# Performance work log

Measured on AMD Instinct MI355X. Metric: run time of the kernel, lower is better.

## Reference

```python
import jax, jax.numpy as jnp
import numpy as np

# --- cfg constants (from init_kwargs) ---
T = 100
DT_MS = 1.0
MAX_RATE_HZ = 200.0
TAU_MEM = 20.0
TAU_PRE = 20.0
TAU_POST = 20.0
V_TH = 16.0
LR_POST = 0.01
LR_PRE = 0.012
W_MAX = 1.0
B, F, N_IN = 256, 1024, 784


def setup_inputs() -> dict:
    key = jax.random.key(0)
    k1, k2, k3 = jax.random.split(key, 3)
    image = jax.random.uniform(k1, (B, 1, 28, 28), dtype=jnp.float32)
    noise = jax.random.uniform(k2, (T, B, 1, 28, 28), dtype=jnp.float32)
    # non-negative excitatory weights, kernel 28x28 flattened -> (F, 784)
    W = jax.random.uniform(k3, (F, N_IN), dtype=jnp.float32) * 0.3
    return {"image": image, "W": W, "noise": noise}


def reference(image, W, noise):
    """Returns spike_count: (B, n_filters)."""
    b = image.shape[0]
    f = W.shape[0]
    # Poisson encoding: P(spike at t) = rate*dt = image * max_rate_hz * dt_ms/1000
    p = image.reshape(b, -1) * (MAX_RATE_HZ * DT_MS / 1000.0)        # (B, 784)
    spikes_in = (noise.reshape(T, b, -1) < p[None]).astype(jnp.float32)  # (T, B, 784)

    decay_mem = jnp.float32(np.exp(-DT_MS / TAU_MEM))
    decay_pre = jnp.float32(np.exp(-DT_MS / TAU_PRE))
    decay_post = jnp.float32(np.exp(-DT_MS / TAU_POST))

    def step(carry, pre):
        mem, w, apre, apost, cnt = carry
        # conv with 28x28 kernel, padding 0 == FC: (B,784) @ (784,F)
        I = pre @ w.T                                   # (B, F)
        mem = mem * decay_mem + I
        spk = (mem >= V_TH).astype(mem.dtype)           # LIF threshold
        mem = mem * (1.0 - spk)                         # reset to 0 on spike
        # --- STDP (pair-based, batch-averaged, Diehl & Cook style) ---
        apre = apre * decay_pre + pre                   # (B, 784) pre trace
        dw_plus = (LR_POST / b) * jnp.einsum('bf,bi->fi', spk, apre)   # LTP on post spike
        dw_minus = (LR_PRE / b) * jnp.einsum('bf,bi->fi', apost, pre)  # LTD on pre spike
        w = jnp.clip(w + dw_plus - dw_minus, 0.0, W_MAX)
        apost = apost * decay_post + spk                # (B, F) post trace
        cnt = cnt + spk
        return (mem, w, apre, apost, cnt), None

    init = (jnp.zeros((b, f), jnp.float32),   # mem
            W,                                 # plastic weights
            jnp.zeros((b, N_IN), jnp.float32), # apre
            jnp.zeros((b, f), jnp.float32),    # apost
            jnp.zeros((b, f), jnp.float32))    # spike_count
    (mem, w, apre, apost, cnt), _ = jax.lax.scan(step, init, spikes_in)
    return cnt
```

## Files before the change

### kernel.cpp

```cpp
#include <hip/hip_runtime.h>
#include <math.h>

#define TSTEPS 100
#define BB 256
#define FF 1024
#define NIN 784
#define NW 13
#define CAPA 192
#define CAPB 128
#define NBLK 1024
#define TPB 256
#define BARSZ 17408

typedef unsigned long long u64;
typedef float f4 __attribute__((ext_vector_type(4)));

__device__ __forceinline__ unsigned at_ld(unsigned* p) {
    return __hip_atomic_load(p, __ATOMIC_RELAXED, __HIP_MEMORY_SCOPE_AGENT);
}
__device__ __forceinline__ void at_st(unsigned* p, unsigned v) {
    __hip_atomic_store(p, v, __ATOMIC_RELAXED, __HIP_MEMORY_SCOPE_AGENT);
}
__device__ __forceinline__ u64 at_ld64(u64* p) {
    return __hip_atomic_load(p, __ATOMIC_RELAXED, __HIP_MEMORY_SCOPE_AGENT);
}
__device__ __forceinline__ void at_st64(u64* p, u64 v) {
    __hip_atomic_store(p, v, __ATOMIC_RELAXED, __HIP_MEMORY_SCOPE_AGENT);
}

__device__ __forceinline__ float sc0_ld(const float* p) {
    float v;
    asm volatile("global_load_dword %0, %1, off sc0\n\t"
                 "s_waitcnt vmcnt(0)"
                 : "=v"(v) : "v"(p) : "memory");
    __builtin_amdgcn_sched_barrier(0);
    return v;
}
__device__ __forceinline__ f4 sc0_ld4(const f4* p) {
    f4 v;
    asm volatile("global_load_dwordx4 %0, %1, off sc0\n\t"
                 "s_waitcnt vmcnt(0)"
                 : "=v"(v) : "v"(p) : "memory");
    __builtin_amdgcn_sched_barrier(0);
    return v;
}
__device__ __forceinline__ void sc0_issue8(
    const float* p0, const float* p1, const float* p2, const float* p3,
    const float* p4, const float* p5, const float* p6, const float* p7,
    float& v0, float& v1, float& v2, float& v3,
    float& v4, float& v5, float& v6, float& v7)
{
    asm volatile(
        "global_load_dword %0, %8, off sc0\n\t"
        "global_load_dword %1, %9, off sc0\n\t"
        "global_load_dword %2, %10, off sc0\n\t"
        "global_load_dword %3, %11, off sc0\n\t"
        "global_load_dword %4, %12, off sc0\n\t"
        "global_load_dword %5, %13, off sc0\n\t"
        "global_load_dword %6, %14, off sc0\n\t"
        "global_load_dword %7, %15, off sc0"
        : "=&v"(v0),"=&v"(v1),"=&v"(v2),"=&v"(v3),
          "=&v"(v4),"=&v"(v5),"=&v"(v6),"=&v"(v7)
        : "v"(p0),"v"(p1),"v"(p2),"v"(p3),"v"(p4),"v"(p5),"v"(p6),"v"(p7)
        : "memory");
}
__device__ __forceinline__ void sc0_ld8(
    const float* p0, const float* p1, const float* p2, const float* p3,
    const float* p4, const float* p5, const float* p6, const float* p7,
    float& v0, float& v1, float& v2, float& v3,
    float& v4, float& v5, float& v6, float& v7)
{
    sc0_issue8(p0,p1,p2,p3,p4,p5,p6,p7, v0,v1,v2,v3,v4,v5,v6,v7);
    asm volatile("s_waitcnt vmcnt(0)" ::: "memory");
    __builtin_amdgcn_sched_barrier(0);
}

template <typename IDX>
__device__ __forceinline__ float foldList(
    const float* __restrict__ base, const IDX* __restrict__ list,
    int k0, int k1, int f)
{
    float c = 0.f;
    int k = k0;
    for (; k + 16 <= k1; k += 16) {
        float v0,v1,v2,v3,v4,v5,v6,v7,v8,v9,v10,v11,v12,v13,v14,v15;
        sc0_issue8(base+((int)list[k+0]<<10)+f, base+((int)list[k+1]<<10)+f,
                   base+((int)list[k+2]<<10)+f, base+((int)list[k+3]<<10)+f,
                   base+((int)list[k+4]<<10)+f, base+((int)list[k+5]<<10)+f,
                   base+((int)list[k+6]<<10)+f, base+((int)list[k+7]<<10)+f,
                   v0,v1,v2,v3,v4,v5,v6,v7);
        sc0_issue8(base+((int)list[k+8]<<10)+f,  base+((int)list[k+9]<<10)+f,
                   base+((int)list[k+10]<<10)+f, base+((int)list[k+11]<<10)+f,
                   base+((int)list[k+12]<<10)+f, base+((int)list[k+13]<<10)+f,
                   base+((int)list[k+14]<<10)+f, base+((int)list[k+15]<<10)+f,
                   v8,v9,v10,v11,v12,v13,v14,v15);
        asm volatile("s_waitcnt vmcnt(0)" ::: "memory");
        __builtin_amdgcn_sched_barrier(0);
        c=__fadd_rn(c,v0);  c=__fadd_rn(c,v1);  c=__fadd_rn(c,v2);  c=__fadd_rn(c,v3);
        c=__fadd_rn(c,v4);  c=__fadd_rn(c,v5);  c=__fadd_rn(c,v6);  c=__fadd_rn(c,v7);
        c=__fadd_rn(c,v8);  c=__fadd_rn(c,v9);  c=__fadd_rn(c,v10); c=__fadd_rn(c,v11);
        c=__fadd_rn(c,v12); c=__fadd_rn(c,v13); c=__fadd_rn(c,v14); c=__fadd_rn(c,v15);
    }
    if (k + 8 <= k1) {
        float v0,v1,v2,v3,v4,v5,v6,v7;
        sc0_ld8(base+((int)list[k+0]<<10)+f, base+((int)list[k+1]<<10)+f,
                base+((int)list[k+2]<<10)+f, base+((int)list[k+3]<<10)+f,
                base+((int)list[k+4]<<10)+f, base+((int)list[k+5]<<10)+f,
                base+((int)list[k+6]<<10)+f, base+((int)list[k+7]<<10)+f,
                v0,v1,v2,v3,v4,v5,v6,v7);
        c=__fadd_rn(c,v0); c=__fadd_rn(c,v1); c=__fadd_rn(c,v2); c=__fadd_rn(c,v3);
        c=__fadd_rn(c,v4); c=__fadd_rn(c,v5); c=__fadd_rn(c,v6); c=__fadd_rn(c,v7);
        k += 8;
    }
    for (; k < k1; ++k)
        c = __fadd_rn(c, sc0_ld(base + ((int)list[k] << 10) + f));
    return c;
}

__global__ __launch_bounds__(256) void k_init(
    const float* __restrict__ W, float* __restrict__ wT,
    float* __restrict__ apreT_g, u64* __restrict__ spkT,
    unsigned* __restrict__ bar)
{
    int idx = blockIdx.x * 256 + threadIdx.x;
    {
        int f = idx & (FF - 1);
        int i = idx >> 10;
        wT[idx] = W[f * NIN + i];
    }
    apreT_g[idx] = 0.f;
    apreT_g[idx + NIN * FF] = 0.f;
    if (idx < 2 * FF * 4) spkT[idx] = 0ull;
    if (idx < BARSZ) bar[idx] = 0u;
}

__global__ __launch_bounds__(256) void k_encode(
    const float* __restrict__ image, const float* __restrict__ noise,
    u64* __restrict__ prebits)
{
    int tid = blockIdx.x * 256 + threadIdx.x;
    int lane = threadIdx.x & 63;
    int word = tid >> 6;
    int wd = word % NW;
    int tb = word / NW;
    int b = tb & (BB - 1);
    int i = (wd << 6) + lane;
    bool s = false;
    if (i < NIN) {
        float pf = __fmul_rn(image[b * NIN + i], 0.2f);
        s = (noise[(size_t)tb * NIN + i] < pf);
    }
    u64 m = __ballot(s);
    if (lane == 0) prebits[word] = m;
}

__global__ __launch_bounds__(256) void k_encode_t(
    const u64* __restrict__ prebits, u64* __restrict__ prebitsT)
{
    int tid = blockIdx.x * 256 + threadIdx.x;
    int b = tid & (BB - 1);
    int ti = tid >> 8;
    int i = ti % NIN;
    int t = ti / NIN;
    u64 w = prebits[((size_t)t * BB + b) * NW + (i >> 6)];
    bool s = (w >> (i & 63)) & 1ull;
    u64 m = __ballot(s);
    if ((threadIdx.x & 63) == 0)
        prebitsT[(size_t)ti * 4 + ((threadIdx.x >> 6) & 3)] = m;
}

__global__ __launch_bounds__(256) void k_lists(
    const u64* __restrict__ prebits, unsigned short* __restrict__ idxA,
    unsigned short* __restrict__ cntA)
{
    int tb = blockIdx.x * 256 + threadIdx.x;
    const u64* pb = prebits + (size_t)tb * NW;
    unsigned short* ia = idxA + (size_t)tb * CAPA;
    int n = 0, c1 = 0, c2 = 0;
    for (int wd = 0; wd < NW; ++wd) {
        u64 m = pb[wd];
        int boff = wd << 6;
        while (m) {
            int j = __builtin_ctzll(m); m &= m - 1;
            if (n < CAPA) ia[n] = (unsigned short)(boff + j);
            ++n;
        }
        if (wd == 5)  c1 = n;
        if (wd == 11) c2 = n;
    }
    if (n > CAPA) n = CAPA;
    if (c2 > n) c2 = n;
    if (c1 > c2) c1 = c2;
    cntA[tb * 4 + 0] = (unsigned short)c1;
    cntA[tb * 4 + 1] = (unsigned short)c2;
    cntA[tb * 4 + 2] = (unsigned short)n;
}

__global__ __launch_bounds__(256) void k_listsT(
    const u64* __restrict__ prebitsT, unsigned char* __restrict__ idxB,
    unsigned short* __restrict__ cntB)
{
    int ti = blockIdx.x * 256 + threadIdx.x;
    if (ti >= TSTEPS * NIN) return;
    const u64* pt = prebitsT + (size_t)ti * 4;
    unsigned char* ib = idxB + (size_t)ti * CAPB;
    int n = 0;
    for (int wb = 0; wb < 4; ++wb) {
        u64 m = pt[wb];
        int boff = wb << 6;
        while (m) {
            int j = __builtin_ctzll(m); m &= m - 1;
            if (n < CAPB) ib[n] = (unsigned char)(boff + j);
            ++n;
        }
    }
    cntB[ti] = (unsigned short)(n > CAPB ? CAPB : n);
}

__global__ __launch_bounds__(TPB, 4) void k_run(
    float* __restrict__ wT, float* __restrict__ apreT_g, float* __restrict__ apost,
    const unsigned short* __restrict__ idxA, const unsigned short* __restrict__ cntA,
    const unsigned char* __restrict__ idxB, const unsigned short* __restrict__ cntB,
    const u64* __restrict__ prebitsT, u64* __restrict__ spkT,
    float* __restrict__ out, unsigned* __restrict__ bar,
    float dmem, float dpre, float dpost, float lrp, float lrm)
{
    __shared__ int shs[16];
    __shared__ int shinfo[4];
    __shared__ unsigned scnt[9];
    __shared__ int sbad;
    __shared__ float sap[4][256];

    const int tix = threadIdx.x;
    const int wv = tix >> 6, lane = tix & 63;
    const int bid = blockIdx.x;

    unsigned* slot = bar;
    if (tix < 9) scnt[tix] = 0u;
    if (tix == 0) {
        unsigned x;
        asm volatile("s_getreg_b32 %0, hwreg(HW_REG_XCC_ID)" : "=s"(x));
        shinfo[0] = (int)(x & 7u);
        at_st(&slot[bid], (x & 7u) + 1u);
    }
    __syncthreads();
    const int xcd = shinfo[0];
    unsigned mv0, mv1, mv2, mv3;
    for (int rounds = 0;; ++rounds) {
        if (tix == 0) sbad = 0;
        __syncthreads();
        mv0 = at_ld(&slot[tix]);
        mv1 = at_ld(&slot[256 + tix]);
        mv2 = at_ld(&slot[512 + tix]);
        mv3 = at_ld(&slot[768 + tix]);
        if (!(mv0 && mv1 && mv2 && mv3)) sbad = 1;
        __syncthreads();
        if (!sbad || rounds > (1 << 20)) break;
        __builtin_amdgcn_s_sleep(2);
    }
    {
        atomicAdd(&scnt[mv0 - 1u], 1u);
        atomicAdd(&scnt[mv1 - 1u], 1u);
        atomicAdd(&scnt[mv2 - 1u], 1u);
        atomicAdd(&scnt[mv3 - 1u], 1u);
        unsigned r = 0;
        if ((int)(mv0 - 1u) == xcd && tix < bid) r++;
        if ((int)(mv1 - 1u) == xcd && 256 + tix < bid) r++;
        if ((int)(mv2 - 1u) == xcd && 512 + tix < bid) r++;
        if ((int)(mv3 - 1u) == xcd && 768 + tix < bid) r++;
        if (r) atomicAdd(&scnt[8], r);
        __syncthreads();
        if (tix == 0) {
            int Kn = 0, gidx = 0;
            for (int x2 = 0; x2 < 8; ++x2)
                if (scnt[x2] > 0) { if (x2 == xcd) gidx = Kn; ++Kn; }
            int ns = 0;
            for (int s = 0; s < 16; ++s)
                if ((s % Kn) == gidx) shs[ns++] = s;
            shinfo[1] = (int)scnt[8];
            shinfo[2] = (int)scnt[xcd];
            shinfo[3] = ns;
        }
        __syncthreads();
    }
    const int rank = shinfo[1], nx = shinfo[2], nsl = shinfo[3];
    const int nxw = nx * 4;
    const int wrank = rank * 4 + wv;
    const int nA = nsl << 8;
    const int nB = nsl * NIN;
    float* apx = apreT_g + (size_t)xcd * (BB * NIN);
    float* sapw = sap[wv];
    unsigned* arrive  = bar + 1024 + xcd * 1024;
    unsigned* release = bar + 9216 + xcd * 1024;
    unsigned ep = 1;

#define A_STATE(Q) float memv##Q = 0.f, cntv##Q = 0.f, apov##Q = 0.f; u64 pbal##Q = 0ull;
    A_STATE(0) A_STATE(1) A_STATE(2) A_STATE(3)

#define DO_A(Q) do { \
    int u = wrank + (Q) * nxw; \
    if (u < nA) { \
        int sl = u >> 8, b = u & 255; \
        int f = (shs[sl] << 6) + lane; \
        apov##Q = __fadd_rn(__fmul_rn(apov##Q, dpost), \
                            (float)((pbal##Q >> lane) & 1ull)); \
        apost[(b << 10) + f] = apov##Q; \
        const unsigned short* ia = idxA + (size_t)(t * BB + b) * CAPA; \
        const unsigned short* ca = cntA + (size_t)(t * BB + b) * 4; \
        int c1 = ca[0], c2 = ca[1], c3 = ca[2]; \
        float I = 0.f; \
        I = __fadd_rn(I, foldList(wT, ia, 0,  c1, f)); \
        I = __fadd_rn(I, foldList(wT, ia, c1, c2, f)); \
        I = __fadd_rn(I, foldList(wT, ia, c2, c3, f)); \
        float mm = __fadd_rn(__fmul_rn(memv##Q, dmem), I); \
        bool spk = (mm >= 16.0f); \
        memv##Q = spk ? 0.f : mm; \
        if (spk) { \
            cntv##Q += 1.f; \
            atomicOr(&cur[(f << 2) | (b >> 6)], 1ull << (b & 63)); \
        } \
        pbal##Q = __ballot(spk); \
    } \
} while (0)

    auto xbar = [&]() {
        asm volatile("s_waitcnt vmcnt(0) lgkmcnt(0)" ::: "memory");
        __syncthreads();
        if (rank == 0) {
            for (int rounds = 0;; ++rounds) {
                if (tix == 0) sbad = 0;
                __syncthreads();
                bool ok = true;
                #pragma unroll
                for (int kk = 0; kk < 4; ++kk) {
                    int r = kk * 256 + tix;
                    if (r < nx && r > 0) ok &= (at_ld(&arrive[r]) >= ep);
                }
                if (!ok) sbad = 1;
                __syncthreads();
                if (!sbad || rounds > (1 << 20)) break;
                __builtin_amdgcn_s_sleep(4);
            }
            #pragma unroll
            for (int kk = 0; kk < 4; ++kk) {
                int r = kk * 256 + tix;
                if (r < nx) at_st(&release[r], ep);
            }
        } else {
            if (tix == 0) {
                at_st(&arrive[rank], ep);
                unsigned spins = 0;
                while (at_ld(&release[rank]) < ep) {
                    if (++spins > (1u << 22)) break;
                    __builtin_amdgcn_s_sleep(8);
                }
            }
            __syncthreads();
        }
        ++ep;
    };

    for (int t = 0; t < TSTEPS; ++t) {
        u64* cur = spkT + (size_t)(t & 1) * (FF * 4);
        u64* nxt = spkT + (size_t)((t + 1) & 1) * (FF * 4);

        DO_A(0); DO_A(1); DO_A(2); DO_A(3);

        for (int r = wrank; r < NIN; r += nxw) {
            const u64* pt = prebitsT + ((size_t)t * NIN + r) * 4;
            u64 w0 = pt[0], w1 = pt[1], w2 = pt[2], w3 = pt[3];
            int bb = lane << 2;
            u64 wsel = (bb & 128) ? ((bb & 64) ? w3 : w2)
                                  : ((bb & 64) ? w1 : w0);
            int s0 = bb & 63;
            f4* vp = (f4*)(apx + ((size_t)r << 8) + bb);
            f4 v = *vp;
            v.x = __fadd_rn(__fmul_rn(v.x, dpre), (float)((wsel >> s0) & 1ull));
            v.y = __fadd_rn(__fmul_rn(v.y, dpre), (float)((wsel >> (s0+1)) & 1ull));
            v.z = __fadd_rn(__fmul_rn(v.z, dpre), (float)((wsel >> (s0+2)) & 1ull));
            v.w = __fadd_rn(__fmul_rn(v.w, dpre), (float)((wsel >> (s0+3)) & 1ull));
            *vp = v;
        }
        for (int wd0 = rank * TPB + tix; wd0 < (nsl << 8); wd0 += nx * TPB) {
            int sl = wd0 >> 8, rest = wd0 & 255;
            int f = (shs[sl] << 6) + (rest >> 2);
            at_st64(&nxt[(f << 2) + (rest & 3)], 0ull);
        }

        if (t == TSTEPS - 1) break;
        xbar();

        for (int q = 0;; ++q) {
            int u = wrank + q * nxw;
            if (u >= nB) break;
            int sl = u / NIN, i = u - sl * NIN;
            int f = (shs[sl] << 6) + lane;

            const unsigned char* ib = idxB + (size_t)(t * NIN + i) * CAPB;
            int cb = cntB[t * NIN + i];
            float Sm = foldList(apost, ib, 0, cb, f);

            asm volatile("s_waitcnt lgkmcnt(0)" ::: "memory");
            __builtin_amdgcn_sched_barrier(0);
            f4 rv = sc0_ld4((const f4*)(apx + ((size_t)i << 8) + (lane << 2)));
            *(f4*)(sapw + (lane << 2)) = rv;
            u64 m0 = at_ld64(&cur[(f << 2) | 0]);
            u64 m1 = at_ld64(&cur[(f << 2) | 1]);
            u64 m2 = at_ld64(&cur[(f << 2) | 2]);
            u64 m3 = at_ld64(&cur[(f << 2) | 3]);
            asm volatile("s_waitcnt lgkmcnt(0)" ::: "memory");
            __builtin_amdgcn_sched_barrier(0);

            float Sp = 0.f;
            u64 m;
            m = m0; while (m) { int j = __builtin_ctzll(m); m &= m - 1;
                                Sp = __fadd_rn(Sp, sapw[j]); }
            m = m1; while (m) { int j = __builtin_ctzll(m); m &= m - 1;
                                Sp = __fadd_rn(Sp, sapw[64 + j]); }
            m = m2; while (m) { int j = __builtin_ctzll(m); m &= m - 1;
                                Sp = __fadd_rn(Sp, sapw[128 + j]); }
            m = m3; while (m) { int j = __builtin_ctzll(m); m &= m - 1;
                                Sp = __fadd_rn(Sp, sapw[192 + j]); }

            int wi = (i << 10) + f;
            float w = wT[wi];
            w = __fadd_rn(w, __fmul_rn(lrp, Sp));
            w = __fsub_rn(w, __fmul_rn(lrm, Sm));
            w = fminf(fmaxf(w, 0.f), 1.f);
            wT[wi] = w;
        }
        xbar();
    }

#define DO_OUT(Q) do { \
    int u = wrank + (Q) * nxw; \
    if (u < nA) { \
        int sl = u >> 8, b = u & 255; \
        int f = (shs[sl] << 6) + lane; \
        out[(b << 10) + f] = cntv##Q; \
    } \
} while (0)
    DO_OUT(0); DO_OUT(1); DO_OUT(2); DO_OUT(3);
}

extern "C" void kernel_launch(void* const* d_in, const int* in_sizes, int n_in,
                              void* d_out, int out_size, void* d_ws, size_t ws_size,
                              hipStream_t stream)
{
    const float* image = (const float*)d_in[0];
    const float* W     = (const float*)d_in[1];
    const float* noise = (const float*)d_in[2];
    float* out = (float*)d_out;

    char* p = (char*)d_ws;
    float* wT      = (float*)p; p += (size_t)NIN * FF * 4;
    float* apreT_g = (float*)p; p += (size_t)8 * BB * NIN * 4;
    float* apost   = (float*)p; p += (size_t)BB * FF * 4;
    u64* prebits   = (u64*)p;   p += (size_t)TSTEPS * BB * NW * 8;
    u64* prebitsT  = (u64*)p;   p += (size_t)TSTEPS * NIN * 4 * 8;
    u64* spkT      = (u64*)p;   p += (size_t)2 * FF * 4 * 8;
    unsigned short* idxA = (unsigned short*)p; p += (size_t)TSTEPS * BB * CAPA * 2;
    unsigned short* cntA = (unsigned short*)p; p += (size_t)TSTEPS * BB * 4 * 2;
    unsigned char*  idxB = (unsigned char*)p;  p += (size_t)TSTEPS * NIN * CAPB;
    unsigned short* cntB = (unsigned short*)p; p += (size_t)TSTEPS * NIN * 2;
    unsigned* bar        = (unsigned*)p;       p += (size_t)BARSZ * 4;

    float dmem = (float)exp(-1.0 / 20.0);
    float dpre = dmem, dpost = dmem;
    float lrp = (float)(0.01 / 256.0);
    float lrm = (float)(0.012 / 256.0);

    k_init<<<(NIN * FF) / 256, 256, 0, stream>>>(W, wT, apreT_g, spkT, bar);
    k_encode<<<(TSTEPS * BB * NW * 64) / 256, 256, 0, stream>>>(image, noise, prebits);
    k_encode_t<<<(TSTEPS * NIN * BB) / 256, 256, 0, stream>>>(prebits, prebitsT);
    k_lists<<<(TSTEPS * BB) / 256, 256, 0, stream>>>(prebits, idxA, cntA);
    k_listsT<<<(TSTEPS * NIN + 255) / 256, 256, 0, stream>>>(prebitsT, idxB, cntB);

    k_run<<<NBLK, TPB, 0, stream>>>(
        wT, apreT_g, apost, idxA, cntA, idxB, cntB,
        prebitsT, spkT, out, bar, dmem, dpre, dpost, lrp, lrm);
}
```

Measured before the change: 4.842 ms.

## Replace atomicOr spike bitmaps with per-wave ballot stores and in-register transpose

```diff
diff --git a/kernel.cpp b/kernel.cpp
--- a/kernel.cpp
+++ b/kernel.cpp
@@ -8,9 +8,9 @@
 #define NW 13
 #define CAPA 192
 #define CAPB 128
-#define NBLK 1024
-#define TPB 256
-#define BARSZ 17408
+#define NBLK 512
+#define TPB 512
+#define BARSZ 8704
 
 typedef unsigned long long u64;
 typedef float f4 __attribute__((ext_vector_type(4)));
@@ -19,12 +19,6 @@
     return __hip_atomic_load(p, __ATOMIC_RELAXED, __HIP_MEMORY_SCOPE_AGENT);
 }
 __device__ __forceinline__ void at_st(unsigned* p, unsigned v) {
-    __hip_atomic_store(p, v, __ATOMIC_RELAXED, __HIP_MEMORY_SCOPE_AGENT);
-}
-__device__ __forceinline__ u64 at_ld64(u64* p) {
-    return __hip_atomic_load(p, __ATOMIC_RELAXED, __HIP_MEMORY_SCOPE_AGENT);
-}
-__device__ __forceinline__ void at_st64(u64* p, u64 v) {
     __hip_atomic_store(p, v, __ATOMIC_RELAXED, __HIP_MEMORY_SCOPE_AGENT);
 }
 
@@ -43,6 +37,20 @@
                  : "=v"(v) : "v"(p) : "memory");
     __builtin_amdgcn_sched_barrier(0);
     return v;
+}
+__device__ __forceinline__ void sc0_ld64x4(
+    const u64* p0, const u64* p1, const u64* p2, const u64* p3,
+    u64& a, u64& b, u64& c, u64& d)
+{
+    asm volatile(
+        "global_load_dwordx2 %0, %4, off sc0\n\t"
+        "global_load_dwordx2 %1, %5, off sc0\n\t"
+        "global_load_dwordx2 %2, %6, off sc0\n\t"
+        "global_load_dwordx2 %3, %7, off sc0\n\t"
+        "s_waitcnt vmcnt(0)"
+        : "=&v"(a),"=&v"(b),"=&v"(c),"=&v"(d)
+        : "v"(p0),"v"(p1),"v"(p2),"v"(p3) : "memory");
+    __builtin_amdgcn_sched_barrier(0);
 }
 __device__ __forceinline__ void sc0_issue8(
     const float* p0, const float* p1, const float* p2, const float* p3,
@@ -119,8 +127,7 @@
 
 __global__ __launch_bounds__(256) void k_init(
     const float* __restrict__ W, float* __restrict__ wT,
-    float* __restrict__ apreT_g, u64* __restrict__ spkT,
-    unsigned* __restrict__ bar)
+    float* __restrict__ apreT_g, unsigned* __restrict__ bar)
 {
     int idx = blockIdx.x * 256 + threadIdx.x;
     {
@@ -130,7 +137,6 @@
     }
     apreT_g[idx] = 0.f;
     apreT_g[idx + NIN * FF] = 0.f;
-    if (idx < 2 * FF * 4) spkT[idx] = 0ull;
     if (idx < BARSZ) bar[idx] = 0u;
 }
 
@@ -217,26 +223,26 @@
     cntB[ti] = (unsigned short)(n > CAPB ? CAPB : n);
 }
 
-__global__ __launch_bounds__(TPB, 4) void k_run(
+__global__ __launch_bounds__(TPB, 2) void k_run(
     float* __restrict__ wT, float* __restrict__ apreT_g, float* __restrict__ apost,
     const unsigned short* __restrict__ idxA, const unsigned short* __restrict__ cntA,
     const unsigned char* __restrict__ idxB, const unsigned short* __restrict__ cntB,
-    const u64* __restrict__ prebitsT, u64* __restrict__ spkT,
+    const u64* __restrict__ prebitsT, u64* __restrict__ spkb,
     float* __restrict__ out, unsigned* __restrict__ bar,
     float dmem, float dpre, float dpost, float lrp, float lrm)
 {
     __shared__ int shs[16];
     __shared__ int shinfo[4];
-    __shared__ unsigned scnt[9];
+    __shared__ unsigned scnt[16];
     __shared__ int sbad;
-    __shared__ float sap[4][256];
+    __shared__ float sap[8][256];
 
     const int tix = threadIdx.x;
     const int wv = tix >> 6, lane = tix & 63;
     const int bid = blockIdx.x;
 
     unsigned* slot = bar;
-    if (tix < 9) scnt[tix] = 0u;
+    if (tix < 16) scnt[tix] = 0u;
     if (tix == 0) {
         unsigned x;
         asm volatile("s_getreg_b32 %0, hwreg(HW_REG_XCC_ID)" : "=s"(x));
@@ -245,53 +251,40 @@
     }
     __syncthreads();
     const int xcd = shinfo[0];
-    unsigned mv0, mv1, mv2, mv3;
+    unsigned mv = 0;
     for (int rounds = 0;; ++rounds) {
         if (tix == 0) sbad = 0;
         __syncthreads();
-        mv0 = at_ld(&slot[tix]);
-        mv1 = at_ld(&slot[256 + tix]);
-        mv2 = at_ld(&slot[512 + tix]);
-        mv3 = at_ld(&slot[768 + tix]);
-        if (!(mv0 && mv1 && mv2 && mv3)) sbad = 1;
+        mv = at_ld(&slot[tix]);
+        if (!mv) sbad = 1;
         __syncthreads();
         if (!sbad || rounds > (1 << 20)) break;
         __builtin_amdgcn_s_sleep(2);
     }
-    {
-        atomicAdd(&scnt[mv0 - 1u], 1u);
-        atomicAdd(&scnt[mv1 - 1u], 1u);
-        atomicAdd(&scnt[mv2 - 1u], 1u);
-        atomicAdd(&scnt[mv3 - 1u], 1u);
-        unsigned r = 0;
-        if ((int)(mv0 - 1u) == xcd && tix < bid) r++;
-        if ((int)(mv1 - 1u) == xcd && 256 + tix < bid) r++;
-        if ((int)(mv2 - 1u) == xcd && 512 + tix < bid) r++;
-        if ((int)(mv3 - 1u) == xcd && 768 + tix < bid) r++;
-        if (r) atomicAdd(&scnt[8], r);
-        __syncthreads();
-        if (tix == 0) {
-            int Kn = 0, gidx = 0;
-            for (int x2 = 0; x2 < 8; ++x2)
-                if (scnt[x2] > 0) { if (x2 == xcd) gidx = Kn; ++Kn; }
-            int ns = 0;
-            for (int s = 0; s < 16; ++s)
-                if ((s % Kn) == gidx) shs[ns++] = s;
-            shinfo[1] = (int)scnt[8];
-            shinfo[2] = (int)scnt[xcd];
-            shinfo[3] = ns;
-        }
-        __syncthreads();
-    }
+    atomicAdd(&scnt[mv - 1u], 1u);
+    if ((int)(mv - 1u) == xcd && tix < bid) atomicAdd(&scnt[8], 1u);
+    __syncthreads();
+    if (tix == 0) {
+        int Kn = 0, gidx = 0;
+        for (int x2 = 0; x2 < 8; ++x2)
+            if (scnt[x2] > 0) { if (x2 == xcd) gidx = Kn; ++Kn; }
+        int ns = 0;
+        for (int s = 0; s < 16; ++s)
+            if ((s % Kn) == gidx) shs[ns++] = s;
+        shinfo[1] = (int)scnt[8];
+        shinfo[2] = (int)scnt[xcd];
+        shinfo[3] = ns;
+    }
+    __syncthreads();
     const int rank = shinfo[1], nx = shinfo[2], nsl = shinfo[3];
-    const int nxw = nx * 4;
-    const int wrank = rank * 4 + wv;
+    const int nxw = nx * 8;
+    const int wrank = rank * 8 + wv;
     const int nA = nsl << 8;
     const int nB = nsl * NIN;
     float* apx = apreT_g + (size_t)xcd * (BB * NIN);
     float* sapw = sap[wv];
-    unsigned* arrive  = bar + 1024 + xcd * 1024;
-    unsigned* release = bar + 9216 + xcd * 1024;
+    unsigned* arrive  = bar + 512 + xcd * 512;
+    unsigned* release = bar + 4608 + xcd * 512;
     unsigned ep = 1;
 
 #define A_STATE(Q) float memv##Q = 0.f, cntv##Q = 0.f, apov##Q = 0.f; u64 pbal##Q = 0ull;
@@ -301,7 +294,8 @@
     int u = wrank + (Q) * nxw; \
     if (u < nA) { \
         int sl = u >> 8, b = u & 255; \
-        int f = (shs[sl] << 6) + lane; \
+        int slice = shs[sl]; \
+        int f = (slice << 6) + lane; \
         apov##Q = __fadd_rn(__fmul_rn(apov##Q, dpost), \
                             (float)((pbal##Q >> lane) & 1ull)); \
         apost[(b << 10) + f] = apov##Q; \
@@ -315,11 +309,9 @@
         float mm = __fadd_rn(__fmul_rn(memv##Q, dmem), I); \
         bool spk = (mm >= 16.0f); \
         memv##Q = spk ? 0.f : mm; \
-        if (spk) { \
-            cntv##Q += 1.f; \
-            atomicOr(&cur[(f << 2) | (b >> 6)], 1ull << (b & 63)); \
-        } \
+        if (spk) cntv##Q += 1.f; \
         pbal##Q = __ballot(spk); \
+        if (lane == 0) spkb[(slice << 8) + b] = pbal##Q;    \
     } \
 } while (0)
 
@@ -330,22 +322,12 @@
             for (int rounds = 0;; ++rounds) {
                 if (tix == 0) sbad = 0;
                 __syncthreads();
-                bool ok = true;
-                #pragma unroll
-                for (int kk = 0; kk < 4; ++kk) {
-                    int r = kk * 256 + tix;
-                    if (r < nx && r > 0) ok &= (at_ld(&arrive[r]) >= ep);
-                }
-                if (!ok) sbad = 1;
+                if (tix > 0 && tix < nx && at_ld(&arrive[tix]) < ep) sbad = 1;
                 __syncthreads();
                 if (!sbad || rounds > (1 << 20)) break;
-                __builtin_amdgcn_s_sleep(4);
+                __builtin_amdgcn_s_sleep(1);
             }
-            #pragma unroll
-            for (int kk = 0; kk < 4; ++kk) {
-                int r = kk * 256 + tix;
-                if (r < nx) at_st(&release[r], ep);
-            }
+            if (tix < nx) at_st(&release[tix], ep);
         } else {
             if (tix == 0) {
                 at_st(&arrive[rank], ep);
@@ -361,9 +343,6 @@
     };
 
     for (int t = 0; t < TSTEPS; ++t) {
-        u64* cur = spkT + (size_t)(t & 1) * (FF * 4);
-        u64* nxt = spkT + (size_t)((t + 1) & 1) * (FF * 4);
-
         DO_A(0); DO_A(1); DO_A(2); DO_A(3);
 
         for (int r = wrank; r < NIN; r += nxw) {
@@ -381,46 +360,55 @@
             v.w = __fadd_rn(__fmul_rn(v.w, dpre), (float)((wsel >> (s0+3)) & 1ull));
             *vp = v;
         }
-        for (int wd0 = rank * TPB + tix; wd0 < (nsl << 8); wd0 += nx * TPB) {
-            int sl = wd0 >> 8, rest = wd0 & 255;
-            int f = (shs[sl] << 6) + (rest >> 2);
-            at_st64(&nxt[(f << 2) + (rest & 3)], 0ull);
-        }
 
         if (t == TSTEPS - 1) break;
         xbar();
 
+        int cursl = -1;
+        u64 tm0 = 0, tm1 = 0, tm2 = 0, tm3 = 0;
         for (int q = 0;; ++q) {
             int u = wrank + q * nxw;
             if (u >= nB) break;
             int sl = u / NIN, i = u - sl * NIN;
-            int f = (shs[sl] << 6) + lane;
+            int slice = shs[sl];
+            int f = (slice << 6) + lane;
+
+            if (sl != cursl) {
+                cursl = sl;
+                const u64* sb = spkb + (slice << 8);
+                u64 v0, v1, v2, v3;
+                sc0_ld64x4(sb + lane, sb + 64 + lane, sb + 128 + lane, sb + 192 + lane,
+                           v0, v1, v2, v3);
+                tm0 = tm1 = tm2 = tm3 = 0ull;
+                #pragma unroll 8
+                for (int fp = 0; fp < 64; ++fp) {
+                    u64 b0 = __ballot((int)((v0 >> fp) & 1ull));
+                    u64 b1 = __ballot((int)((v1 >> fp) & 1ull));
+                    u64 b2 = __ballot((int)((v2 >> fp) & 1ull));
+                    u64 b3 = __ballot((int)((v3 >> fp) & 1ull));
+                    if (lane == fp) { tm0 = b0; tm1 = b1; tm2 = b2; tm3 = b3; }
+                }
+            }
 
             const unsigned char* ib = idxB + (size_t)(t * NIN + i) * CAPB;
             int cb = cntB[t * NIN + i];
             float Sm = foldList(apost, ib, 0, cb, f);
 
+            f4 rv = sc0_ld4((const f4*)(apx + ((size_t)i << 8) + (lane << 2)));
+            *(f4*)(sapw + (lane << 2)) = rv;
             asm volatile("s_waitcnt lgkmcnt(0)" ::: "memory");
             __builtin_amdgcn_sched_barrier(0);
-            f4 rv = sc0_ld4((const f4*)(apx + ((size_t)i << 8) + (lane << 2)));
-            *(f4*)(sapw + (lane << 2)) = rv;
-            u64 m0 = at_ld64(&cur[(f << 2) | 0]);
-            u64 m1 = at_ld64(&cur[(f << 2) | 1]);
-            u64 m2 = at_ld64(&cur[(f << 2) | 2]);
-            u64 m3 = at_ld64(&cur[(f << 2) | 3]);
-            asm volatile("s_waitcnt lgkmcnt(0)" ::: "memory");
-            __builtin_amdgcn_sched_barrier(0);
 
             float Sp = 0.f;
             u64 m;
-            m = m0; while (m) { int j = __builtin_ctzll(m); m &= m - 1;
-                                Sp = __fadd_rn(Sp, sapw[j]); }
-            m = m1; while (m) { int j = __builtin_ctzll(m); m &= m - 1;
-                                Sp = __fadd_rn(Sp, sapw[64 + j]); }
-            m = m2; while (m) { int j = __builtin_ctzll(m); m &= m - 1;
-                                Sp = __fadd_rn(Sp, sapw[128 + j]); }
-            m = m3; while (m) { int j = __builtin_ctzll(m); m &= m - 1;
-                                Sp = __fadd_rn(Sp, sapw[192 + j]); }
+            m = tm0; while (m) { int j = __builtin_ctzll(m); m &= m - 1;
+                                 Sp = __fadd_rn(Sp, sapw[j]); }
+            m = tm1; while (m) { int j = __builtin_ctzll(m); m &= m - 1;
+                                 Sp = __fadd_rn(Sp, sapw[64 + j]); }
+            m = tm2; while (m) { int j = __builtin_ctzll(m); m &= m - 1;
+                                 Sp = __fadd_rn(Sp, sapw[128 + j]); }
+            m = tm3; while (m) { int j = __builtin_ctzll(m); m &= m - 1;
+                                 Sp = __fadd_rn(Sp, sapw[192 + j]); }
 
             int wi = (i << 10) + f;
             float w = wT[wi];
@@ -458,7 +446,7 @@
     float* apost   = (float*)p; p += (size_t)BB * FF * 4;
     u64* prebits   = (u64*)p;   p += (size_t)TSTEPS * BB * NW * 8;
     u64* prebitsT  = (u64*)p;   p += (size_t)TSTEPS * NIN * 4 * 8;
-    u64* spkT      = (u64*)p;   p += (size_t)2 * FF * 4 * 8;
+    u64* spkb      = (u64*)p;   p += (size_t)16 * 256 * 8;
     unsigned short* idxA = (unsigned short*)p; p += (size_t)TSTEPS * BB * CAPA * 2;
     unsigned short* cntA = (unsigned short*)p; p += (size_t)TSTEPS * BB * 4 * 2;
     unsigned char*  idxB = (unsigned char*)p;  p += (size_t)TSTEPS * NIN * CAPB;
@@ -470,7 +458,7 @@
     float lrp = (float)(0.01 / 256.0);
     float lrm = (float)(0.012 / 256.0);
 
-    k_init<<<(NIN * FF) / 256, 256, 0, stream>>>(W, wT, apreT_g, spkT, bar);
+    k_init<<<(NIN * FF) / 256, 256, 0, stream>>>(W, wT, apreT_g, bar);
     k_encode<<<(TSTEPS * BB * NW * 64) / 256, 256, 0, stream>>>(image, noise, prebits);
     k_encode_t<<<(TSTEPS * NIN * BB) / 256, 256, 0, stream>>>(prebits, prebitsT);
     k_lists<<<(TSTEPS * BB) / 256, 256, 0, stream>>>(prebits, idxA, cntA);
@@ -478,5 +466,5 @@
 
     k_run<<<NBLK, TPB, 0, stream>>>(
         wT, apreT_g, apost, idxA, cntA, idxB, cntB,
-        prebitsT, spkT, out, bar, dmem, dpre, dpost, lrp, lrm);
-}
+        prebitsT, spkb, out, bar, dmem, dpre, dpost, lrp, lrm);
+}
```

After: 6.374 ms. 31.6% more time.
